# Performance work log

Hardware: AMD Instinct MI355X
Metric: run time of the kernel (lower is better)

## Reference

```python
import jax, jax.numpy as jnp
import numpy as np
from functools import partial

WINDOW = 2048
STEP = WINDOW // 2
N_COEFFS = WINDOW // 2 + 1
CPD = 64  # control_plane_dim


def _hann(n):
    # torch.hann_window default is periodic
    return 0.5 - 0.5 * jnp.cos(2.0 * jnp.pi * jnp.arange(n) / n)


def setup_inputs() -> dict:
    key = jax.random.key(0)
    k1, k2, k3 = jax.random.split(key, 3)
    batch, time = 4, 65536
    x = jax.random.normal(k1, (batch, CPD, time), dtype=jnp.float32)
    # stable recurrence: |transfer| < 1
    transfer = jax.random.uniform(k2, (CPD, N_COEFFS), dtype=jnp.float32) * 0.8
    mixer_matrix = jnp.eye(CPD, dtype=jnp.float32) + 0.05 * jax.random.normal(k3, (CPD, CPD), dtype=jnp.float32)
    gain = jnp.ones((1,), dtype=jnp.float32)
    return {"x": x, "transfer": transfer, "mixer_matrix": mixer_matrix, "gain": gain}


def reference(x, transfer, mixer_matrix, gain):
    batch, channels, time = x.shape
    # (x.permute(0,2,1) @ M).permute(0,2,1)
    x = jnp.einsum('bct,cd->bdt', x, mixer_matrix)

    # windowed_audio: pad by step, unfold, apply hann window
    window = _hann(WINDOW).astype(x.dtype)
    xp = jnp.pad(x, ((0, 0), (0, 0), (0, STEP)))
    padded_len = xp.shape[-1]
    frames = (padded_len - WINDOW) // STEP + 1
    idx = jnp.arange(frames)[:, None] * STEP + jnp.arange(WINDOW)[None, :]  # [frames, window]
    windowed = xp[:, :, idx] * window  # [b, c, frames, window]

    spec = jnp.fft.rfft(windowed, axis=-1)  # [b, c, frames, n_coeffs] complex

    # recurrence: out[i] = (spec[i] + out[i-1]) * transfer
    T = transfer[None, :, :]  # broadcast over batch within a frame [1, c, coeffs]

    def step(carry, s):
        out = (s + carry) * T
        return out, out

    spec_f = jnp.moveaxis(spec, 2, 0)  # [frames, b, c, coeffs]
    init = jnp.zeros_like(spec_f[0])
    _, outs = jax.lax.scan(step, init, spec_f)
    output = jnp.moveaxis(outs, 0, 2)  # [b, c, frames, coeffs]

    audio_windows = jnp.fft.irfft(output, n=WINDOW, axis=-1)
    # overlap_add with apply_window=True
    audio_windows = audio_windows * window
    total = (frames - 1) * STEP + WINDOW
    flat_idx = idx.reshape(-1)
    samples = jnp.zeros((batch, channels, total), dtype=x.dtype)
    samples = samples.at[:, :, flat_idx].add(audio_windows.reshape(batch, channels, -1))

    samples = samples * gain
    samples = jnp.tanh(samples)
    return samples[..., :time]
```

## Files before the change

### kernel.cpp

```cpp
#include <hip/hip_runtime.h>
#include <math.h>

#define TIME_N 65536
#define HALFN  1024
#define NBINS  1025
#define NFRAMES 64
#define FCHUNK 8
#define NCHUNK (NFRAMES / FCHUNK)

#define TT 128
__global__ __launch_bounds__(256) void mix_kernel(const float* __restrict__ x,
                                                  const float* __restrict__ M,
                                                  float* __restrict__ out) {
    __shared__ float Ml[64 * 64];
    __shared__ float xt[64][136];
    const int b   = blockIdx.y;
    const int t0  = blockIdx.x * TT;
    const int tid = threadIdx.x;

    for (int i = tid; i < 64 * 64; i += 256) Ml[i] = M[i];

    for (int r = 0; r < 8; ++r) {
        int fi = tid + r * 256;
        int c  = fi >> 5;
        int t4 = fi & 31;
        float4 v = *reinterpret_cast<const float4*>(
            x + (size_t)(b * 64 + c) * TIME_N + t0 + t4 * 4);
        *reinterpret_cast<float4*>(&xt[c][t4 * 4]) = v;
    }
    __syncthreads();

    const int dq = tid >> 5;
    const int tq = tid & 31;

    float acc[8][4];
#pragma unroll
    for (int i = 0; i < 8; ++i)
#pragma unroll
        for (int j = 0; j < 4; ++j) acc[i][j] = 0.f;

    for (int c = 0; c < 64; ++c) {
        float xv[4];
#pragma unroll
        for (int j = 0; j < 4; ++j) xv[j] = xt[c][tq + 32 * j];
#pragma unroll
        for (int i = 0; i < 8; ++i) {
            float mv = Ml[c * 64 + dq * 8 + i];
#pragma unroll
            for (int j = 0; j < 4; ++j) acc[i][j] += xv[j] * mv;
        }
    }

#pragma unroll
    for (int i = 0; i < 8; ++i) {
        int d = dq * 8 + i;
        size_t baseo = (size_t)(b * 64 + d) * TIME_N + t0;
#pragma unroll
        for (int j = 0; j < 4; ++j) out[baseo + tq + 32 * j] = acc[i][j];
    }
}

__device__ __forceinline__ int P(int i) { return i + (i >> 4); }
#define BUFSZ 1088

__device__ __forceinline__ float2 cadd(float2 a, float2 b){return make_float2(a.x+b.x, a.y+b.y);}
__device__ __forceinline__ float2 csub(float2 a, float2 b){return make_float2(a.x-b.x, a.y-b.y);}
__device__ __forceinline__ float2 cmul(float2 a, float2 b){return make_float2(a.x*b.x - a.y*b.y, a.x*b.y + a.y*b.x);}

__device__ __forceinline__ float ftanh(float x) {
    float ax = fabsf(x);
    float e  = __expf(-2.0f * ax);
    float t  = (1.0f - e) * __builtin_amdgcn_rcpf(1.0f + e);
    return copysignf(t, x);
}

template<int SGN>
__device__ __forceinline__ void dft4(float2 x0, float2 x1, float2 x2, float2 x3,
                                     float2& y0, float2& y1, float2& y2, float2& y3) {
    float2 apc = cadd(x0, x2), amc = csub(x0, x2);
    float2 bpd = cadd(x1, x3), bmd = csub(x1, x3);
    float2 sj  = make_float2(-(float)SGN * bmd.y, (float)SGN * bmd.x);
    y0 = cadd(apc, bpd);
    y1 = cadd(amc, sj);
    y2 = csub(apc, bpd);
    y3 = csub(amc, sj);
}

template<int SGN>
__device__ __forceinline__ void dft16_tw(const float2 (&x)[16], float2 w, float2 (&z)[16]) {
    const float S = (float)SGN;
    const float2 K1 = make_float2( 0.9238795325112867f, S * 0.3826834323650898f);
    const float2 K2 = make_float2( 0.7071067811865476f, S * 0.7071067811865476f);
    const float2 K3 = make_float2( 0.3826834323650898f, S * 0.9238795325112867f);
    const float2 K6 = make_float2(-0.7071067811865476f, S * 0.7071067811865476f);
    const float2 K9 = make_float2(-0.9238795325112867f, -S * 0.3826834323650898f);
    float2 u[16];
    {
        float2 y0, y1, y2, y3;
        dft4<SGN>(x[0], x[4], x[8],  x[12], y0, y1, y2, y3);
        u[0]=y0; u[1]=y1; u[2]=y2; u[3]=y3;
        dft4<SGN>(x[1], x[5], x[9],  x[13], y0, y1, y2, y3);
        u[4]=y0; u[5]=cmul(y1,K1); u[6]=cmul(y2,K2); u[7]=cmul(y3,K3);
        dft4<SGN>(x[2], x[6], x[10], x[14], y0, y1, y2, y3);
        u[8]=y0; u[9]=cmul(y1,K2);
        u[10]=make_float2(-S*y2.y, S*y2.x);
        u[11]=cmul(y3,K6);
        dft4<SGN>(x[3], x[7], x[11], x[15], y0, y1, y2, y3);
        u[12]=y0; u[13]=cmul(y1,K3); u[14]=cmul(y2,K6); u[15]=cmul(y3,K9);
    }
    float2 w2 = cmul(w,  w);
    float2 w3 = cmul(w2, w);
    float2 w4 = cmul(w2, w2);
    float2 w8 = cmul(w4, w4);
    float2 w12 = cmul(w8, w4);
#pragma unroll
    for (int i = 0; i < 4; ++i) {
        float2 y0, y1, y2, y3;
        dft4<SGN>(u[i], u[i+4], u[i+8], u[i+12], y0, y1, y2, y3);
        float2 t1 = cmul(y1, w4), t2 = cmul(y2, w8), t3 = cmul(y3, w12);
        if (i == 0) { z[0] = y0; z[4] = t1; z[8] = t2; z[12] = t3; }
        else {
            float2 wl = (i == 1) ? w : ((i == 2) ? w2 : w3);
            z[i]      = cmul(y0, wl);
            z[i + 4]  = cmul(t1, wl);
            z[i + 8]  = cmul(t2, wl);
            z[i + 12] = cmul(t3, wl);
        }
    }
}

template<int SGN, int S>
__device__ __forceinline__ void stage16(const float2* __restrict__ src,
                                        float2* __restrict__ dst,
                                        const float2* __restrict__ twl,
                                        int lane) {
    const int p = lane / S;
    const int q = lane - p * S;
    float2 x[16];
#pragma unroll
    for (int m = 0; m < 16; ++m) x[m] = src[P(lane + 64 * m)];
    float2 w = twl[S * p];
    if (SGN > 0) w.y = -w.y;
    float2 z[16];
    dft16_tw<SGN>(x, w, z);
#pragma unroll
    for (int m = 0; m < 16; ++m) dst[P(q + 16 * S * p + S * m)] = z[m];
}

template<int SGN>
__device__ __forceinline__ void stage4(float2* __restrict__ buf, int lt) {
#pragma unroll
    for (int r = 0; r < 4; ++r) {
        int i = lt + 64 * r;
        float2 a = buf[P(i)], b = buf[P(i + 256)], c = buf[P(i + 512)], d = buf[P(i + 768)];
        float2 y0, y1, y2, y3;
        dft4<SGN>(a, b, c, d, y0, y1, y2, y3);
        buf[P(i)]       = y0;
        buf[P(i + 256)] = y1;
        buf[P(i + 512)] = y2;
        buf[P(i + 768)] = y3;
    }
}

__global__ __launch_bounds__(512) void stft_chain_kernel(
    const float* __restrict__ transfer,
    const float* __restrict__ gainp,
    float* __restrict__ io)
{
    __shared__ float2 bufs[2][FCHUNK][BUFSZ];
    __shared__ float2 tailbuf[2][512];
    __shared__ float2 twl[64];
    __shared__ float2 win2[512];

    const int bd  = blockIdx.x;
    const int d   = bd & 63;
    const int tid = threadIdx.x;
    const int lf  = tid >> 6;
    const int lt  = tid & 63;
    const float g = gainp[0];
    const size_t base = (size_t)bd * TIME_N;
    const float PI  = 3.14159265358979323846f;
    const float PI2 = 6.2831853071795864769f;
    const float inv = 1.0f / 1024.0f;

    const int kb = (tid == 0) ? 1024 : 1024 - tid;
    const float T0 = transfer[(size_t)d * NBINS + tid];
    const float T1 = transfer[(size_t)d * NBINS + kb];
    const float T5 = (tid == 0) ? transfer[(size_t)d * NBINS + 512] : 0.f;
    float2 C0 = make_float2(0.f, 0.f);
    float2 C1 = make_float2(0.f, 0.f);
    float2 C5 = make_float2(0.f, 0.f);
    float sHt, cHt; __sincosf((PI / HALFN) * (float)tid, &sHt, &cHt);

    tailbuf[0][tid] = make_float2(0.f, 0.f);
    tailbuf[1][tid] = make_float2(0.f, 0.f);
    if (tid < 64) {
        float s_, c_; __sincosf(-(PI2 / 1024.0f) * (float)tid, &s_, &c_);
        twl[tid] = make_float2(c_, s_);
    }
    {
        const float cd = __cosf(PI / 1024.0f);
        const float sd = __sinf(PI / 1024.0f);
        float s0, c0; __sincosf((PI / 512.0f) * (float)tid, &s0, &c0);
        float c1 = c0 * cd - s0 * sd;
        win2[tid] = make_float2(0.5f - 0.5f * c0, 0.5f - 0.5f * c1);
    }
    __syncthreads();

    for (int ch = 0; ch < NCHUNK; ++ch) {
        const int par = ch & 1;

        {
            const int tb = (ch * FCHUNK + lf) * HALFN;
            float2 x[16];
#pragma unroll
            for (int m = 0; m < 16; ++m) {
                int n = lt + 64 * m;
                int t = tb + 2 * n;
                float2 v = make_float2(0.f, 0.f);
                if (t < TIME_N)
                    v = *reinterpret_cast<const float2*>(io + base + t);
                float2 wv;
                if (m < 8) wv = win2[n];
                else { float2 ww = win2[n - 512]; wv = make_float2(1.f - ww.x, 1.f - ww.y); }
                x[m] = make_float2(v.x * wv.x, v.y * wv.y);
            }
            float2 w = twl[lt];
            float2 z[16];
            dft16_tw<-1>(x, w, z);
            float2* dst = &bufs[0][lf][0];
#pragma unroll
            for (int m = 0; m < 16; ++m) dst[P(16 * lt + m)] = z[m];
        }
        stage16<-1, 16>(&bufs[0][lf][0], &bufs[1][lf][0], twl, lt);
        stage4<-1>(&bufs[1][lf][0], lt);

        __syncthreads();

        {
            float2 Zk = bufs[1][0][P(tid)];
            float2 Zn = bufs[1][0][P((HALFN - tid) & (HALFN - 1))];
#pragma unroll 2
            for (int f = 0; f < FCHUNK; ++f) {
                float2 Zk_n, Zn_n;
                if (f < FCHUNK - 1) {
                    Zk_n = bufs[1][f + 1][P(tid)];
                    Zn_n = bufs[1][f + 1][P((HALFN - tid) & (HALFN - 1))];
                }
                float2 Fe = make_float2(0.5f * (Zk.x + Zn.x), 0.5f * (Zk.y - Zn.y));
                float2 Fo = make_float2(0.5f * (Zk.y + Zn.y), -0.5f * (Zk.x - Zn.x));
                float2 U  = cmul(make_float2(cHt, -sHt), Fo);
                C0.x = (Fe.x + U.x + C0.x) * T0;
                C0.y = (Fe.y + U.y + C0.y) * T0;
                C1.x = (Fe.x - U.x + C1.x) * T1;
                C1.y = (U.y - Fe.y + C1.y) * T1;
                float2 Fe2 = make_float2(0.5f * (C0.x + C1.x), 0.5f * (C0.y - C1.y));
                float2 num = make_float2(0.5f * (C0.x - C1.x), 0.5f * (C0.y + C1.y));
                float2 Fo2 = cmul(make_float2(cHt, sHt), num);
                bufs[1][f][P(tid)] = make_float2(Fe2.x - Fo2.y, Fe2.y + Fo2.x);
                if (tid != 0) {
                    bufs[1][f][P(HALFN - tid)] =
                        make_float2(Fe2.x + Fo2.y, Fo2.x - Fe2.y);
                } else {
                    float2 Z5 = bufs[1][f][P(512)];
                    C5.x = ( Z5.x + C5.x) * T5;
                    C5.y = (-Z5.y + C5.y) * T5;
                    bufs[1][f][P(512)] = make_float2(C5.x, -C5.y);
                }
                Zk = Zk_n; Zn = Zn_n;
            }
        }
        __syncthreads();

        stage16<1, 1>(&bufs[1][lf][0], &bufs[0][lf][0], twl, lt);
        stage16<1, 16>(&bufs[0][lf][0], &bufs[1][lf][0], twl, lt);
        stage4<1>(&bufs[1][lf][0], lt);

        if (lf == 7) {
#pragma unroll 2
            for (int j = 0; j < 8; ++j) {
                int m = lt + 64 * j;
                tailbuf[par][m] = bufs[1][7][P(m + 512)];
            }
        }
        __syncthreads();

        {
            const int tb = (ch * FCHUNK + lf) * HALFN;
#pragma unroll 2
            for (int j = 0; j < 8; ++j) {
                int m = lt + 64 * j;
                float2 z  = bufs[1][lf][P(m)];
                float2 zp = (lf == 0) ? tailbuf[par ^ 1][m]
                                      : bufs[1][lf - 1][P(m + 512)];
                float2 wf = win2[m];
                float y0 = inv * (z.x * wf.x + zp.x * (1.f - wf.x));
                float y1 = inv * (z.y * wf.y + zp.y * (1.f - wf.y));
                float2 o = make_float2(ftanh(g * y0), ftanh(g * y1));
                *reinterpret_cast<float2*>(io + base + tb + 2 * m) = o;
            }
        }
        __syncthreads();
    }
}

extern "C" void kernel_launch(void* const* d_in, const int* in_sizes, int n_in,
                              void* d_out, int out_size, void* d_ws, size_t ws_size,
                              hipStream_t stream) {
    const float* x        = (const float*)d_in[0];
    const float* transfer = (const float*)d_in[1];
    const float* mixer    = (const float*)d_in[2];
    const float* gain     = (const float*)d_in[3];
    float* out = (float*)d_out;

    dim3 g1(TIME_N / TT, 4);
    mix_kernel<<<g1, 256, 0, stream>>>(x, mixer, out);

    stft_chain_kernel<<<256, 512, 0, stream>>>(transfer, gain, out);
}
```

Measured before the change: 136.8 us.

## Run FFT stages in place and process 16 frames per chunk

Replaces the ping-pong shared buffers with a single in-place buffer, so each wave of 64 lanes transforms its frame without a second copy. The freed LDS is used to double the frames per chunk to 16, with each wave handling two frames, which halves the number of chunk iterations and their block-wide barriers. In exchange each wave does twice the serial work per phase, and the in-place stages depend on a compiler memory barrier to keep every load ahead of the stores, which is fragile.

```diff
diff --git a/kernel.cpp b/kernel.cpp
--- a/kernel.cpp
+++ b/kernel.cpp
@@ -5,7 +5,7 @@
 #define HALFN  1024
 #define NBINS  1025
 #define NFRAMES 64
-#define FCHUNK 8
+#define FCHUNK 16
 #define NCHUNK (NFRAMES / FCHUNK)
 
 #define TT 128
@@ -130,25 +130,25 @@
 }
 
 template<int SGN, int S>
-__device__ __forceinline__ void stage16(const float2* __restrict__ src,
-                                        float2* __restrict__ dst,
-                                        const float2* __restrict__ twl,
-                                        int lane) {
+__device__ __forceinline__ void stage16_ip(float2* __restrict__ b,
+                                           const float2* __restrict__ twl,
+                                           int lane) {
     const int p = lane / S;
     const int q = lane - p * S;
     float2 x[16];
 #pragma unroll
-    for (int m = 0; m < 16; ++m) x[m] = src[P(lane + 64 * m)];
+    for (int m = 0; m < 16; ++m) x[m] = b[P(lane + 64 * m)];
+    asm volatile("" ::: "memory");
     float2 w = twl[S * p];
     if (SGN > 0) w.y = -w.y;
     float2 z[16];
     dft16_tw<SGN>(x, w, z);
 #pragma unroll
-    for (int m = 0; m < 16; ++m) dst[P(q + 16 * S * p + S * m)] = z[m];
+    for (int m = 0; m < 16; ++m) b[P(q + 16 * S * p + S * m)] = z[m];
 }
 
 template<int SGN>
-__device__ __forceinline__ void stage4(float2* __restrict__ buf, int lt) {
+__device__ __forceinline__ void stage4_ip(float2* __restrict__ buf, int lt) {
 #pragma unroll
     for (int r = 0; r < 4; ++r) {
         int i = lt + 64 * r;
@@ -167,7 +167,7 @@
     const float* __restrict__ gainp,
     float* __restrict__ io)
 {
-    __shared__ float2 bufs[2][FCHUNK][BUFSZ];
+    __shared__ float2 buf[FCHUNK][BUFSZ];
     __shared__ float2 tailbuf[2][512];
     __shared__ float2 twl[64];
     __shared__ float2 win2[512];
@@ -210,42 +210,45 @@
     for (int ch = 0; ch < NCHUNK; ++ch) {
         const int par = ch & 1;
 
+#pragma unroll
+        for (int fl = 0; fl < 2; ++fl) {
+            const int f  = 2 * lf + fl;
+            const int tb = (ch * FCHUNK + f) * HALFN;
+            {
+                float2 x[16];
+#pragma unroll
+                for (int m = 0; m < 16; ++m) {
+                    int n = lt + 64 * m;
+                    int t = tb + 2 * n;
+                    float2 v = make_float2(0.f, 0.f);
+                    if (t < TIME_N)
+                        v = *reinterpret_cast<const float2*>(io + base + t);
+                    float2 wv;
+                    if (m < 8) wv = win2[n];
+                    else { float2 ww = win2[n - 512]; wv = make_float2(1.f - ww.x, 1.f - ww.y); }
+                    x[m] = make_float2(v.x * wv.x, v.y * wv.y);
+                }
+                float2 w = twl[lt];
+                float2 z[16];
+                dft16_tw<-1>(x, w, z);
+                float2* dst = &buf[f][0];
+#pragma unroll
+                for (int m = 0; m < 16; ++m) dst[P(16 * lt + m)] = z[m];
+            }
+            stage16_ip<-1, 16>(&buf[f][0], twl, lt);
+            stage4_ip<-1>(&buf[f][0], lt);
+        }
+        __syncthreads();
+
         {
-            const int tb = (ch * FCHUNK + lf) * HALFN;
-            float2 x[16];
-#pragma unroll
-            for (int m = 0; m < 16; ++m) {
-                int n = lt + 64 * m;
-                int t = tb + 2 * n;
-                float2 v = make_float2(0.f, 0.f);
-                if (t < TIME_N)
-                    v = *reinterpret_cast<const float2*>(io + base + t);
-                float2 wv;
-                if (m < 8) wv = win2[n];
-                else { float2 ww = win2[n - 512]; wv = make_float2(1.f - ww.x, 1.f - ww.y); }
-                x[m] = make_float2(v.x * wv.x, v.y * wv.y);
-            }
-            float2 w = twl[lt];
-            float2 z[16];
-            dft16_tw<-1>(x, w, z);
-            float2* dst = &bufs[0][lf][0];
-#pragma unroll
-            for (int m = 0; m < 16; ++m) dst[P(16 * lt + m)] = z[m];
-        }
-        stage16<-1, 16>(&bufs[0][lf][0], &bufs[1][lf][0], twl, lt);
-        stage4<-1>(&bufs[1][lf][0], lt);
-
-        __syncthreads();
-
-        {
-            float2 Zk = bufs[1][0][P(tid)];
-            float2 Zn = bufs[1][0][P((HALFN - tid) & (HALFN - 1))];
+            float2 Zk = buf[0][P(tid)];
+            float2 Zn = buf[0][P((HALFN - tid) & (HALFN - 1))];
 #pragma unroll 2
             for (int f = 0; f < FCHUNK; ++f) {
                 float2 Zk_n, Zn_n;
                 if (f < FCHUNK - 1) {
-                    Zk_n = bufs[1][f + 1][P(tid)];
-                    Zn_n = bufs[1][f + 1][P((HALFN - tid) & (HALFN - 1))];
+                    Zk_n = buf[f + 1][P(tid)];
+                    Zn_n = buf[f + 1][P((HALFN - tid) & (HALFN - 1))];
                 }
                 float2 Fe = make_float2(0.5f * (Zk.x + Zn.x), 0.5f * (Zk.y - Zn.y));
                 float2 Fo = make_float2(0.5f * (Zk.y + Zn.y), -0.5f * (Zk.x - Zn.x));
@@ -257,42 +260,48 @@
                 float2 Fe2 = make_float2(0.5f * (C0.x + C1.x), 0.5f * (C0.y - C1.y));
                 float2 num = make_float2(0.5f * (C0.x - C1.x), 0.5f * (C0.y + C1.y));
                 float2 Fo2 = cmul(make_float2(cHt, sHt), num);
-                bufs[1][f][P(tid)] = make_float2(Fe2.x - Fo2.y, Fe2.y + Fo2.x);
+                buf[f][P(tid)] = make_float2(Fe2.x - Fo2.y, Fe2.y + Fo2.x);
                 if (tid != 0) {
-                    bufs[1][f][P(HALFN - tid)] =
+                    buf[f][P(HALFN - tid)] =
                         make_float2(Fe2.x + Fo2.y, Fo2.x - Fe2.y);
                 } else {
-                    float2 Z5 = bufs[1][f][P(512)];
+                    float2 Z5 = buf[f][P(512)];
                     C5.x = ( Z5.x + C5.x) * T5;
                     C5.y = (-Z5.y + C5.y) * T5;
-                    bufs[1][f][P(512)] = make_float2(C5.x, -C5.y);
+                    buf[f][P(512)] = make_float2(C5.x, -C5.y);
                 }
                 Zk = Zk_n; Zn = Zn_n;
             }
         }
         __syncthreads();
 
-        stage16<1, 1>(&bufs[1][lf][0], &bufs[0][lf][0], twl, lt);
-        stage16<1, 16>(&bufs[0][lf][0], &bufs[1][lf][0], twl, lt);
-        stage4<1>(&bufs[1][lf][0], lt);
+#pragma unroll
+        for (int fl = 0; fl < 2; ++fl) {
+            const int f = 2 * lf + fl;
+            stage16_ip<1, 1>(&buf[f][0], twl, lt);
+            stage16_ip<1, 16>(&buf[f][0], twl, lt);
+            stage4_ip<1>(&buf[f][0], lt);
+        }
 
         if (lf == 7) {
 #pragma unroll 2
             for (int j = 0; j < 8; ++j) {
                 int m = lt + 64 * j;
-                tailbuf[par][m] = bufs[1][7][P(m + 512)];
+                tailbuf[par][m] = buf[FCHUNK - 1][P(m + 512)];
             }
         }
         __syncthreads();
 
-        {
-            const int tb = (ch * FCHUNK + lf) * HALFN;
+#pragma unroll
+        for (int fl = 0; fl < 2; ++fl) {
+            const int f  = 2 * lf + fl;
+            const int tb = (ch * FCHUNK + f) * HALFN;
 #pragma unroll 2
             for (int j = 0; j < 8; ++j) {
                 int m = lt + 64 * j;
-                float2 z  = bufs[1][lf][P(m)];
-                float2 zp = (lf == 0) ? tailbuf[par ^ 1][m]
-                                      : bufs[1][lf - 1][P(m + 512)];
+                float2 z  = buf[f][P(m)];
+                float2 zp = (f == 0) ? tailbuf[par ^ 1][m]
+                                     : buf[f - 1][P(m + 512)];
                 float2 wf = win2[m];
                 float y0 = inv * (z.x * wf.x + zp.x * (1.f - wf.x));
                 float y1 = inv * (z.y * wf.y + zp.y * (1.f - wf.y));
```

After: 134.1 us. 2.0% less time.
